# Kernel optimization log

Hardware: AMD Instinct MI355X
Metric: run time of the kernel (lower is better)

The kernel has to match this reference:

```python
import jax, jax.numpy as jnp
import numpy as np

N = 50000       # nodes
E = 800000      # edges
F_IN = 128      # input node features
F_OUT = 16      # per-head output features
H = 8           # attention heads
SLOPE = 0.2     # LeakyReLU negative slope


def setup_inputs() -> dict:
    key = jax.random.key(0)
    k1, k2, k3, k4 = jax.random.split(key, 4)
    node_features = jax.random.normal(k1, (N, F_IN), dtype=jnp.float32)
    edge_index = jax.random.randint(k2, (2, E), 0, N, dtype=jnp.int32)
    # target_w = neighbor_w (share_weights=True): Linear(F_IN -> H*F_OUT) with bias
    W = jax.random.normal(k3, (H * F_OUT, F_IN), dtype=jnp.float32) / np.float32(np.sqrt(F_IN))
    b = jnp.zeros((H * F_OUT,), dtype=jnp.float32)
    # attn = Linear(2*F_OUT -> 1, bias=False); store as vector a of length 2*F_OUT
    a = jax.random.normal(k4, (2 * F_OUT,), dtype=jnp.float32) / np.float32(np.sqrt(2 * F_OUT))
    return {"node_features": node_features, "edge_index": edge_index, "W": W, "b": b, "a": a}


def reference(node_features, edge_index, W, b, a):
    src = edge_index[0]  # neighbor nodes j
    tgt = edge_index[1]  # target nodes i
    # shared projection (share_weights=True): project once per node, then gather per edge
    h = (node_features @ W.T + b).reshape(N, H, F_OUT)  # [N, H, F_OUT]
    h_i = h[tgt]  # [E, H, F_OUT]
    h_j = h[src]  # [E, H, F_OUT]
    # attn applied to concat([h_i, h_j]) == h_i @ a[:F_OUT] + h_j @ a[F_OUT:]
    e = jnp.einsum('ehf,f->eh', h_i, a[:F_OUT]) + jnp.einsum('ehf,f->eh', h_j, a[F_OUT:])
    e = jnp.where(e > 0, e, SLOPE * e)  # LeakyReLU
    # scatter_softmax over incoming edges of each target node (per head)
    seg_max = jax.ops.segment_max(e, tgt, num_segments=N)        # [N, H]
    ex = jnp.exp(e - seg_max[tgt])                               # [E, H]
    denom = jax.ops.segment_sum(ex, tgt, num_segments=N)         # [N, H]
    alpha = ex / denom[tgt]                                      # [E, H]
    # message = alpha * h_j, skip connection adds h_i per edge (as in source)
    msg = alpha[..., None] * h_j + h_i                           # [E, H, F_OUT]
    out = jax.ops.segment_sum(msg, tgt, num_segments=N)          # [N, H, F_OUT]
    out = out.reshape(N, H * F_OUT)                              # concat heads
    return jax.nn.elu(out)
```

## Files before the change

### kernel.cpp

```cpp
#include <hip/hip_runtime.h>
#include <hip/hip_fp16.h>
#include <cmath>

#define NN 50000
#define NE 800000
#define SLOPE 0.2f
#define NTILES 782
#define DSTRIDE 64

#define NBKT 196
#define NCHK 196
#define BINCAP 64

#define OFF_H    0
#define OFF_H8   3200000
#define OFF_AL   4800000
#define OFF_AR   5200000
#define OFF_CUR  5600000
#define OFF_CSR  5650000
#define OFF_BKT  7250000
#define OFF_CNTS 9708624

using half8   = __attribute__((ext_vector_type(8))) _Float16;
using floatx4 = __attribute__((ext_vector_type(4))) float;
using floatx2 = __attribute__((ext_vector_type(2))) float;
using intx4   = __attribute__((ext_vector_type(4))) int;

#define WST 136

__global__ __launch_bounds__(256) void project_bin_kernel(
    const float* __restrict__ X,
    const float* __restrict__ W,
    const float* __restrict__ Bv,
    const float* __restrict__ Av,
    const int* __restrict__ ei,
    __half* __restrict__ h, unsigned char* __restrict__ h8,
    float* __restrict__ al, float* __restrict__ ar,
    unsigned* __restrict__ bkt, unsigned* __restrict__ cnts)
{
    __shared__ _Float16 Wh[128 * WST];
    __shared__ _Float16 Cs[64 * WST];
    __shared__ float As[32];
    __shared__ unsigned bincnt[NBKT];
    const int tid = threadIdx.x;
    const int bid = blockIdx.x;

    if (bid >= NTILES) {
        const int c = bid - NTILES;
        if (tid < NBKT) bincnt[tid] = 0;
        __syncthreads();
#pragma unroll
        for (int it = 0; it < 4; ++it) {
            const int e0 = c * 4096 + tid * 4 + it * 1024;
            if (e0 < NE) {
                intx4 tg = *(const intx4*)(ei + NE + e0);
                intx4 sr = *(const intx4*)(ei + e0);
#pragma unroll
                for (int k = 0; k < 4; ++k) {
                    unsigned p = ((unsigned)tg[k] << 16) | (unsigned)sr[k];
                    unsigned b = p >> 24;
                    unsigned slot = atomicAdd(&bincnt[b], 1u);
                    if (slot < BINCAP)
                        bkt[(((unsigned)c * NBKT + b) << 6) + slot] = p;
                }
            }
        }
        __syncthreads();
        if (tid < NBKT) cnts[c * NBKT + tid] = bincnt[tid];
        return;
    }

    for (int i = tid; i < 128 * 128; i += 256) {
        int o = i >> 7, k = i & 127;
        Wh[o * WST + k] = (_Float16)W[i];
    }
    if (tid < 32) As[tid] = Av[tid];
    __syncthreads();

    const int wave = tid >> 6;
    const int lane = tid & 63;
    const int q = lane >> 4;
    const int n = lane & 15;
    const int gn = bid * 64 + wave * 16 + n;
    const bool valid = gn < NN;
    const float* xrow = X + ((long)gn << 7);

    half8 afrag[4];
#pragma unroll
    for (int kc = 0; kc < 4; ++kc) {
        float4 x0 = make_float4(0.f, 0.f, 0.f, 0.f), x1 = x0;
        if (valid) {
            x0 = *(const float4*)(xrow + kc * 32 + q * 8);
            x1 = *(const float4*)(xrow + kc * 32 + q * 8 + 4);
        }
        half8 a;
        a[0] = (_Float16)x0.x; a[1] = (_Float16)x0.y;
        a[2] = (_Float16)x0.z; a[3] = (_Float16)x0.w;
        a[4] = (_Float16)x1.x; a[5] = (_Float16)x1.y;
        a[6] = (_Float16)x1.z; a[7] = (_Float16)x1.w;
        afrag[kc] = a;
    }

    floatx4 acc[8];
#pragma unroll
    for (int nt = 0; nt < 8; ++nt) {
        float b = Bv[nt * 16 + n];
        acc[nt][0] = b; acc[nt][1] = b; acc[nt][2] = b; acc[nt][3] = b;
    }
#pragma unroll
    for (int nt = 0; nt < 8; ++nt) {
        const _Float16* wrow = &Wh[(nt * 16 + n) * WST];
#pragma unroll
        for (int kc = 0; kc < 4; ++kc) {
            half8 bfrag = *(const half8*)(wrow + kc * 32 + q * 8);
            acc[nt] = __builtin_amdgcn_mfma_f32_16x16x32_f16(afrag[kc], bfrag, acc[nt], 0, 0, 0);
        }
    }

    _Float16* cw = &Cs[(wave * 16) * WST];
#pragma unroll
    for (int nt = 0; nt < 8; ++nt) {
#pragma unroll
        for (int r = 0; r < 4; ++r) {
            cw[(q * 4 + r) * WST + nt * 16 + n] = (_Float16)acc[nt][r];
        }
    }
    __syncthreads();

    {
        int rw = tid >> 2, ch = tid & 3;
        int gnode = bid * 64 + rw;
        if (gnode < NN) {
            const uint4* src = (const uint4*)&Cs[rw * WST + ch * 32];
            uint4 v[4] = { src[0], src[1], src[2], src[3] };
            uint4* dst = (uint4*)&h[((long)gnode << 7) + ch * 32];
            dst[0] = v[0]; dst[1] = v[1]; dst[2] = v[2]; dst[3] = v[3];

            const unsigned int* dw = (const unsigned int*)v;
            unsigned int res[8];
#pragma unroll
            for (int w = 0; w < 8; ++w) {
                unsigned int lo = dw[2 * w], hi = dw[2 * w + 1];
                float2 f0 = __half22float2(*(const __half2*)&lo);
                float2 f1 = __half22float2(*(const __half2*)&hi);
                unsigned int r = 0;
                r = __builtin_amdgcn_cvt_pk_fp8_f32(f0.x, f0.y, r, false);
                r = __builtin_amdgcn_cvt_pk_fp8_f32(f1.x, f1.y, r, true);
                res[w] = r;
            }
            uint4* d8 = (uint4*)&h8[((long)gnode << 7) + ch * 32];
            d8[0] = make_uint4(res[0], res[1], res[2], res[3]);
            d8[1] = make_uint4(res[4], res[5], res[6], res[7]);
        }
    }
    for (int p = tid; p < 512; p += 256) {
        int nd = p >> 3, hh = p & 7;
        int gnode = bid * 64 + nd;
        if (gnode >= NN) continue;
        const _Float16* c = &Cs[nd * WST + hh * 16];
        float pL = 0.f, pR = 0.f;
#pragma unroll
        for (int f = 0; f < 16; ++f) {
            float hv = (float)c[f];
            pL = fmaf(hv, As[f], pL);
            pR = fmaf(hv, As[16 + f], pR);
        }
        al[gnode * 8 + hh] = pL;
        ar[gnode * 8 + hh] = pR;
    }
}

__global__ __launch_bounds__(512) void csr_kernel(
    const unsigned* __restrict__ bkt, const unsigned* __restrict__ cnts,
    int* __restrict__ cur, unsigned short* __restrict__ csr)
{
    __shared__ unsigned short csl[256 * DSTRIDE];
    __shared__ unsigned cnt256[256];
    __shared__ unsigned segcnt[NBKT];
    const int tid = threadIdx.x, bin = blockIdx.x;
    if (tid < 256) cnt256[tid] = 0;
    if (tid < NBKT) segcnt[tid] = cnts[tid * NBKT + bin];
    __syncthreads();

    const int w = tid >> 6, lane = tid & 63;
    for (int s = w; s < NCHK; s += 8) {
        unsigned m = min(segcnt[s], (unsigned)BINCAP);
        if ((unsigned)lane < m) {
            unsigned p = bkt[(((unsigned)s * NBKT + bin) << 6) + lane];
            unsigned local = (p >> 16) & 255u;
            unsigned slot = atomicAdd(&cnt256[local], 1u);
            if (slot < DSTRIDE) csl[(local << 6) + slot] = (unsigned short)(p & 0xFFFFu);
        }
    }
    __syncthreads();

    if (tid < 256) {
        const int gnode = bin * 256 + tid;
        if (gnode < NN) cur[gnode] = (int)cnt256[tid];
    }
    const int nrows = min(256, NN - bin * 256);
    uint4* dst = (uint4*)(csr + ((size_t)bin << 14));
    const uint4* srcp = (const uint4*)csl;
    for (int i = tid; i < nrows * 8; i += 512) dst[i] = srcp[i];
}

#define ARLD(s) (*(const float*)((const char*)ar + ((((unsigned)(s)) << 5) | arof)))
#define CSRLD(o) (*(const unsigned short*)((const char*)csr + (o)))
#define CVTLO(w) __builtin_amdgcn_cvt_pk_f32_fp8((unsigned short)(w), false)
#define CVTHI(w) __builtin_amdgcn_cvt_pk_f32_fp8((unsigned short)((w) >> 16), false)

__global__ __launch_bounds__(256) void gather_kernel(
    const int* __restrict__ cur, const unsigned short* __restrict__ csr,
    const float* __restrict__ al, const float* __restrict__ ar,
    const __half* __restrict__ h, const unsigned char* __restrict__ h8,
    float* __restrict__ out)
{
    const int wid = threadIdx.x >> 6;
    const int n = blockIdx.x * 4 + wid;
    if (n >= NN) return;
    const int lane = threadIdx.x & 63;
    const int c2 = lane << 1;
    const int hh = lane >> 3;
    const int el = lane & 7;
    const int deg = cur[n];
    const int degc = min(deg, DSTRIDE);
    const unsigned cbase = ((unsigned)n) << 7;
    const unsigned arof = ((unsigned)hh) << 2;
    const unsigned hof = ((unsigned)hh) << 4;
    const float aLt = al[n * 8 + hh];

    floatx2 a0 = {0.f,0.f}, a1 = a0, a2 = a0, a3 = a0, a4 = a0, a5 = a0, a6 = a0, a7 = a0;
    float den = 0.f;

    for (int j = 0; j < degc; j += 16) {
        const bool va = (j + el) < degc;
        const bool vb = (j + 8 + el) < degc;
        const unsigned co = cbase + (((unsigned)(j + el)) << 1);
        int ms0 = va ? (int)CSRLD(co) : 0;
        int ms1 = vb ? (int)CSRLD(co + 16u) : 0;
        float v0 = aLt + ARLD(ms0);
        float v1 = aLt + ARLD(ms1);
        v0 = v0 > 0.0f ? v0 : SLOPE * v0;
        v1 = v1 > 0.0f ? v1 : SLOPE * v1;
        float me0 = va ? __expf(fminf(v0, 60.0f)) : 0.0f;
        float me1 = vb ? __expf(fminf(v1, 60.0f)) : 0.0f;
        uint4 A = *(const uint4*)(h8 + ((((unsigned)ms0) << 7) | hof));
        uint4 B = *(const uint4*)(h8 + ((((unsigned)ms1) << 7) | hof));
        den += me0 + me1;
        a0 += CVTLO(A.x) * me0; a1 += CVTHI(A.x) * me0;
        a2 += CVTLO(A.y) * me0; a3 += CVTHI(A.y) * me0;
        a4 += CVTLO(A.z) * me0; a5 += CVTHI(A.z) * me0;
        a6 += CVTLO(A.w) * me0; a7 += CVTHI(A.w) * me0;
        a0 += CVTLO(B.x) * me1; a1 += CVTHI(B.x) * me1;
        a2 += CVTLO(B.y) * me1; a3 += CVTHI(B.y) * me1;
        a4 += CVTLO(B.z) * me1; a5 += CVTHI(B.z) * me1;
        a6 += CVTLO(B.w) * me1; a7 += CVTHI(B.w) * me1;
    }

    {
        floatx2 v0_ = (el & 4) ? a0 : a4;
        floatx2 v1_ = (el & 4) ? a1 : a5;
        floatx2 v2_ = (el & 4) ? a2 : a6;
        floatx2 v3_ = (el & 4) ? a3 : a7;
        floatx2 o0 = (el & 4) ? a4 : a0;
        floatx2 o1 = (el & 4) ? a5 : a1;
        floatx2 o2 = (el & 4) ? a6 : a2;
        floatx2 o3 = (el & 4) ? a7 : a3;
        o0[0] += __shfl_xor(v0_[0], 4); o0[1] += __shfl_xor(v0_[1], 4);
        o1[0] += __shfl_xor(v1_[0], 4); o1[1] += __shfl_xor(v1_[1], 4);
        o2[0] += __shfl_xor(v2_[0], 4); o2[1] += __shfl_xor(v2_[1], 4);
        o3[0] += __shfl_xor(v3_[0], 4); o3[1] += __shfl_xor(v3_[1], 4);
        floatx2 w0 = (el & 2) ? o0 : o2;
        floatx2 w1 = (el & 2) ? o1 : o3;
        floatx2 p0 = (el & 2) ? o2 : o0;
        floatx2 p1 = (el & 2) ? o3 : o1;
        p0[0] += __shfl_xor(w0[0], 2); p0[1] += __shfl_xor(w0[1], 2);
        p1[0] += __shfl_xor(w1[0], 2); p1[1] += __shfl_xor(w1[1], 2);
        floatx2 z = (el & 1) ? p0 : p1;
        floatx2 fin = (el & 1) ? p1 : p0;
        fin[0] += __shfl_xor(z[0], 1); fin[1] += __shfl_xor(z[1], 1);
        a0 = fin;
    }
    den += __shfl_xor(den, 1);
    den += __shfl_xor(den, 2);
    den += __shfl_xor(den, 4);

    unsigned hv = __builtin_nontemporal_load(
        (const unsigned*)((const char*)h + (((size_t)n) << 8) + ((unsigned)c2 << 1)));
    float2 hs = __half22float2(*(const __half2*)&hv);
    float degf = (float)deg;
    float inv = (den > 0.0f) ? 1.0f / den : 0.0f;
    float o0 = fmaf(degf, hs.x, a0[0] * inv);
    float o1 = fmaf(degf, hs.y, a0[1] * inv);
    o0 = o0 > 0.0f ? o0 : __expf(o0) - 1.0f;
    o1 = o1 > 0.0f ? o1 : __expf(o1) - 1.0f;
    floatx2 res = {o0, o1};
    __builtin_nontemporal_store(res,
        (floatx2*)((char*)out + (((size_t)n) << 9) + ((unsigned)c2 << 2)));
}

extern "C" void kernel_launch(void* const* d_in, const int* in_sizes, int n_in,
                              void* d_out, int out_size, void* d_ws, size_t ws_size,
                              hipStream_t stream) {
    const float* X = (const float*)d_in[0];
    const int* ei  = (const int*)d_in[1];
    const float* W = (const float*)d_in[2];
    const float* B = (const float*)d_in[3];
    const float* A = (const float*)d_in[4];
    float* ws  = (float*)d_ws;
    __half* h  = (__half*)(ws + OFF_H);
    unsigned char* h8 = (unsigned char*)(ws + OFF_H8);
    float* al  = ws + OFF_AL;
    float* ar  = ws + OFF_AR;
    int* cur   = (int*)ws + OFF_CUR;
    unsigned short* csr = (unsigned short*)(ws + OFF_CSR);
    unsigned* bkt  = (unsigned*)(ws + OFF_BKT);
    unsigned* cnts = (unsigned*)(ws + OFF_CNTS);
    float* out = (float*)d_out;

    project_bin_kernel<<<NTILES + NCHK, 256, 0, stream>>>(X, W, B, A, ei, h, h8, al, ar, bkt, cnts);
    csr_kernel<<<NBKT, 512, 0, stream>>>(bkt, cnts, cur, csr);
    gather_kernel<<<(NN + 3) / 4, 256, 0, stream>>>(cur, csr, al, ar, h, h8, out);
}
```

Before: 139.6 us.

## Fuse CSR build into gather kernel using shared-memory adjacency per 32-node slice

Merges the CSR construction and gather kernels into one. Each of 8 blocks per 256-node bin rebuilds its 32-node neighbor lists in shared memory, then its waves run the softmax-weighted aggregation straight from LDS. This removes a kernel launch and the global CSR/degree write and read-back. In exchange each bucket entry is read 8 times (once per block in the bin), and each wave handles 8 nodes serially with fewer blocks overall.

```diff
diff --git a/kernel.cpp b/kernel.cpp
--- a/kernel.cpp
+++ b/kernel.cpp
@@ -16,8 +16,6 @@
 #define OFF_H8   3200000
 #define OFF_AL   4800000
 #define OFF_AR   5200000
-#define OFF_CUR  5600000
-#define OFF_CSR  5650000
 #define OFF_BKT  7250000
 #define OFF_CNTS 9708624
 
@@ -170,133 +168,123 @@
     }
 }
 
-__global__ __launch_bounds__(512) void csr_kernel(
+#define ARLD(s) (*(const float*)((const char*)ar + ((((unsigned)(s)) << 5) | arof)))
+#define CVTLO(w) __builtin_amdgcn_cvt_pk_f32_fp8((unsigned short)(w), false)
+#define CVTHI(w) __builtin_amdgcn_cvt_pk_f32_fp8((unsigned short)((w) >> 16), false)
+
+__global__ __launch_bounds__(256) void csr_gather_kernel(
     const unsigned* __restrict__ bkt, const unsigned* __restrict__ cnts,
-    int* __restrict__ cur, unsigned short* __restrict__ csr)
+    const float* __restrict__ al, const float* __restrict__ ar,
+    const __half* __restrict__ h, const unsigned char* __restrict__ h8,
+    float* __restrict__ out)
 {
-    __shared__ unsigned short csl[256 * DSTRIDE];
-    __shared__ unsigned cnt256[256];
+    __shared__ unsigned short csl[32 * DSTRIDE];
+    __shared__ unsigned cnt[32];
     __shared__ unsigned segcnt[NBKT];
-    const int tid = threadIdx.x, bin = blockIdx.x;
-    if (tid < 256) cnt256[tid] = 0;
+    const int tid = threadIdx.x;
+    const int bin = blockIdx.x >> 3;
+    const int o   = blockIdx.x & 7;
+    if (tid < 32) cnt[tid] = 0;
     if (tid < NBKT) segcnt[tid] = cnts[tid * NBKT + bin];
     __syncthreads();
 
     const int w = tid >> 6, lane = tid & 63;
-    for (int s = w; s < NCHK; s += 8) {
+    for (int s = w; s < NCHK; s += 4) {
         unsigned m = min(segcnt[s], (unsigned)BINCAP);
         if ((unsigned)lane < m) {
             unsigned p = bkt[(((unsigned)s * NBKT + bin) << 6) + lane];
             unsigned local = (p >> 16) & 255u;
-            unsigned slot = atomicAdd(&cnt256[local], 1u);
-            if (slot < DSTRIDE) csl[(local << 6) + slot] = (unsigned short)(p & 0xFFFFu);
+            if ((local >> 5) == (unsigned)o) {
+                unsigned idx = local & 31u;
+                unsigned slot = atomicAdd(&cnt[idx], 1u);
+                if (slot < DSTRIDE) csl[(idx << 6) + slot] = (unsigned short)(p & 0xFFFFu);
+            }
         }
     }
     __syncthreads();
 
-    if (tid < 256) {
-        const int gnode = bin * 256 + tid;
-        if (gnode < NN) cur[gnode] = (int)cnt256[tid];
-    }
-    const int nrows = min(256, NN - bin * 256);
-    uint4* dst = (uint4*)(csr + ((size_t)bin << 14));
-    const uint4* srcp = (const uint4*)csl;
-    for (int i = tid; i < nrows * 8; i += 512) dst[i] = srcp[i];
-}
-
-#define ARLD(s) (*(const float*)((const char*)ar + ((((unsigned)(s)) << 5) | arof)))
-#define CSRLD(o) (*(const unsigned short*)((const char*)csr + (o)))
-#define CVTLO(w) __builtin_amdgcn_cvt_pk_f32_fp8((unsigned short)(w), false)
-#define CVTHI(w) __builtin_amdgcn_cvt_pk_f32_fp8((unsigned short)((w) >> 16), false)
-
-__global__ __launch_bounds__(256) void gather_kernel(
-    const int* __restrict__ cur, const unsigned short* __restrict__ csr,
-    const float* __restrict__ al, const float* __restrict__ ar,
-    const __half* __restrict__ h, const unsigned char* __restrict__ h8,
-    float* __restrict__ out)
-{
-    const int wid = threadIdx.x >> 6;
-    const int n = blockIdx.x * 4 + wid;
-    if (n >= NN) return;
-    const int lane = threadIdx.x & 63;
     const int c2 = lane << 1;
     const int hh = lane >> 3;
     const int el = lane & 7;
-    const int deg = cur[n];
-    const int degc = min(deg, DSTRIDE);
-    const unsigned cbase = ((unsigned)n) << 7;
     const unsigned arof = ((unsigned)hh) << 2;
-    const unsigned hof = ((unsigned)hh) << 4;
-    const float aLt = al[n * 8 + hh];
-
-    floatx2 a0 = {0.f,0.f}, a1 = a0, a2 = a0, a3 = a0, a4 = a0, a5 = a0, a6 = a0, a7 = a0;
-    float den = 0.f;
-
-    for (int j = 0; j < degc; j += 16) {
-        const bool va = (j + el) < degc;
-        const bool vb = (j + 8 + el) < degc;
-        const unsigned co = cbase + (((unsigned)(j + el)) << 1);
-        int ms0 = va ? (int)CSRLD(co) : 0;
-        int ms1 = vb ? (int)CSRLD(co + 16u) : 0;
-        float v0 = aLt + ARLD(ms0);
-        float v1 = aLt + ARLD(ms1);
-        v0 = v0 > 0.0f ? v0 : SLOPE * v0;
-        v1 = v1 > 0.0f ? v1 : SLOPE * v1;
-        float me0 = va ? __expf(fminf(v0, 60.0f)) : 0.0f;
-        float me1 = vb ? __expf(fminf(v1, 60.0f)) : 0.0f;
-        uint4 A = *(const uint4*)(h8 + ((((unsigned)ms0) << 7) | hof));
-        uint4 B = *(const uint4*)(h8 + ((((unsigned)ms1) << 7) | hof));
-        den += me0 + me1;
-        a0 += CVTLO(A.x) * me0; a1 += CVTHI(A.x) * me0;
-        a2 += CVTLO(A.y) * me0; a3 += CVTHI(A.y) * me0;
-        a4 += CVTLO(A.z) * me0; a5 += CVTHI(A.z) * me0;
-        a6 += CVTLO(A.w) * me0; a7 += CVTHI(A.w) * me0;
-        a0 += CVTLO(B.x) * me1; a1 += CVTHI(B.x) * me1;
-        a2 += CVTLO(B.y) * me1; a3 += CVTHI(B.y) * me1;
-        a4 += CVTLO(B.z) * me1; a5 += CVTHI(B.z) * me1;
-        a6 += CVTLO(B.w) * me1; a7 += CVTHI(B.w) * me1;
-    }
-
-    {
-        floatx2 v0_ = (el & 4) ? a0 : a4;
-        floatx2 v1_ = (el & 4) ? a1 : a5;
-        floatx2 v2_ = (el & 4) ? a2 : a6;
-        floatx2 v3_ = (el & 4) ? a3 : a7;
-        floatx2 o0 = (el & 4) ? a4 : a0;
-        floatx2 o1 = (el & 4) ? a5 : a1;
-        floatx2 o2 = (el & 4) ? a6 : a2;
-        floatx2 o3 = (el & 4) ? a7 : a3;
-        o0[0] += __shfl_xor(v0_[0], 4); o0[1] += __shfl_xor(v0_[1], 4);
-        o1[0] += __shfl_xor(v1_[0], 4); o1[1] += __shfl_xor(v1_[1], 4);
-        o2[0] += __shfl_xor(v2_[0], 4); o2[1] += __shfl_xor(v2_[1], 4);
-        o3[0] += __shfl_xor(v3_[0], 4); o3[1] += __shfl_xor(v3_[1], 4);
-        floatx2 w0 = (el & 2) ? o0 : o2;
-        floatx2 w1 = (el & 2) ? o1 : o3;
-        floatx2 p0 = (el & 2) ? o2 : o0;
-        floatx2 p1 = (el & 2) ? o3 : o1;
-        p0[0] += __shfl_xor(w0[0], 2); p0[1] += __shfl_xor(w0[1], 2);
-        p1[0] += __shfl_xor(w1[0], 2); p1[1] += __shfl_xor(w1[1], 2);
-        floatx2 z = (el & 1) ? p0 : p1;
-        floatx2 fin = (el & 1) ? p1 : p0;
-        fin[0] += __shfl_xor(z[0], 1); fin[1] += __shfl_xor(z[1], 1);
-        a0 = fin;
-    }
-    den += __shfl_xor(den, 1);
-    den += __shfl_xor(den, 2);
-    den += __shfl_xor(den, 4);
-
-    unsigned hv = __builtin_nontemporal_load(
-        (const unsigned*)((const char*)h + (((size_t)n) << 8) + ((unsigned)c2 << 1)));
-    float2 hs = __half22float2(*(const __half2*)&hv);
-    float degf = (float)deg;
-    float inv = (den > 0.0f) ? 1.0f / den : 0.0f;
-    float o0 = fmaf(degf, hs.x, a0[0] * inv);
-    float o1 = fmaf(degf, hs.y, a0[1] * inv);
-    o0 = o0 > 0.0f ? o0 : __expf(o0) - 1.0f;
-    o1 = o1 > 0.0f ? o1 : __expf(o1) - 1.0f;
-    floatx2 res = {o0, o1};
-    __builtin_nontemporal_store(res,
-        (floatx2*)((char*)out + (((size_t)n) << 9) + ((unsigned)c2 << 2)));
+    const unsigned hof  = ((unsigned)hh) << 4;
+
+    for (int t = 0; t < 8; ++t) {
+        const int idx = w * 8 + t;
+        const int n = bin * 256 + o * 32 + idx;
+        if (n >= NN) break;
+        const int deg = (int)cnt[idx];
+        const int degc = min(deg, DSTRIDE);
+        const float aLt = al[n * 8 + hh];
+        unsigned hv = __builtin_nontemporal_load(
+            (const unsigned*)((const char*)h + (((size_t)n) << 8) + ((unsigned)c2 << 1)));
+        const unsigned short* srcl = &csl[idx << 6];
+
+        floatx2 a0 = {0.f,0.f}, a1 = a0, a2 = a0, a3 = a0, a4 = a0, a5 = a0, a6 = a0, a7 = a0;
+        float den = 0.f;
+        for (int j = 0; j < degc; j += 16) {
+            const bool va = (j + el) < degc;
+            const bool vb = (j + 8 + el) < degc;
+            int ms0 = va ? (int)srcl[j + el] : 0;
+            int ms1 = vb ? (int)srcl[j + 8 + el] : 0;
+            float v0 = aLt + ARLD(ms0);
+            float v1 = aLt + ARLD(ms1);
+            v0 = v0 > 0.0f ? v0 : SLOPE * v0;
+            v1 = v1 > 0.0f ? v1 : SLOPE * v1;
+            float me0 = va ? __expf(fminf(v0, 60.0f)) : 0.0f;
+            float me1 = vb ? __expf(fminf(v1, 60.0f)) : 0.0f;
+            uint4 A = *(const uint4*)(h8 + ((((unsigned)ms0) << 7) | hof));
+            uint4 B = *(const uint4*)(h8 + ((((unsigned)ms1) << 7) | hof));
+            den += me0 + me1;
+            a0 += CVTLO(A.x) * me0; a1 += CVTHI(A.x) * me0;
+            a2 += CVTLO(A.y) * me0; a3 += CVTHI(A.y) * me0;
+            a4 += CVTLO(A.z) * me0; a5 += CVTHI(A.z) * me0;
+            a6 += CVTLO(A.w) * me0; a7 += CVTHI(A.w) * me0;
+            a0 += CVTLO(B.x) * me1; a1 += CVTHI(B.x) * me1;
+            a2 += CVTLO(B.y) * me1; a3 += CVTHI(B.y) * me1;
+            a4 += CVTLO(B.z) * me1; a5 += CVTHI(B.z) * me1;
+            a6 += CVTLO(B.w) * me1; a7 += CVTHI(B.w) * me1;
+        }
+
+        {
+            floatx2 v0_ = (el & 4) ? a0 : a4;
+            floatx2 v1_ = (el & 4) ? a1 : a5;
+            floatx2 v2_ = (el & 4) ? a2 : a6;
+            floatx2 v3_ = (el & 4) ? a3 : a7;
+            floatx2 o0 = (el & 4) ? a4 : a0;
+            floatx2 o1 = (el & 4) ? a5 : a1;
+            floatx2 o2 = (el & 4) ? a6 : a2;
+            floatx2 o3 = (el & 4) ? a7 : a3;
+            o0[0] += __shfl_xor(v0_[0], 4); o0[1] += __shfl_xor(v0_[1], 4);
+            o1[0] += __shfl_xor(v1_[0], 4); o1[1] += __shfl_xor(v1_[1], 4);
+            o2[0] += __shfl_xor(v2_[0], 4); o2[1] += __shfl_xor(v2_[1], 4);
+            o3[0] += __shfl_xor(v3_[0], 4); o3[1] += __shfl_xor(v3_[1], 4);
+            floatx2 w0 = (el & 2) ? o0 : o2;
+            floatx2 w1 = (el & 2) ? o1 : o3;
+            floatx2 p0 = (el & 2) ? o2 : o0;
+            floatx2 p1 = (el & 2) ? o3 : o1;
+            p0[0] += __shfl_xor(w0[0], 2); p0[1] += __shfl_xor(w0[1], 2);
+            p1[0] += __shfl_xor(w1[0], 2); p1[1] += __shfl_xor(w1[1], 2);
+            floatx2 z = (el & 1) ? p0 : p1;
+            floatx2 fin = (el & 1) ? p1 : p0;
+            fin[0] += __shfl_xor(z[0], 1); fin[1] += __shfl_xor(z[1], 1);
+            a0 = fin;
+        }
+        den += __shfl_xor(den, 1);
+        den += __shfl_xor(den, 2);
+        den += __shfl_xor(den, 4);
+
+        float2 hs = __half22float2(*(const __half2*)&hv);
+        float degf = (float)deg;
+        float inv = (den > 0.0f) ? 1.0f / den : 0.0f;
+        float o0v = fmaf(degf, hs.x, a0[0] * inv);
+        float o1v = fmaf(degf, hs.y, a0[1] * inv);
+        o0v = o0v > 0.0f ? o0v : __expf(o0v) - 1.0f;
+        o1v = o1v > 0.0f ? o1v : __expf(o1v) - 1.0f;
+        floatx2 res = {o0v, o1v};
+        __builtin_nontemporal_store(res,
+            (floatx2*)((char*)out + (((size_t)n) << 9) + ((unsigned)c2 << 2)));
+    }
 }
 
 extern "C" void kernel_launch(void* const* d_in, const int* in_sizes, int n_in,
@@ -312,13 +300,10 @@
     unsigned char* h8 = (unsigned char*)(ws + OFF_H8);
     float* al  = ws + OFF_AL;
     float* ar  = ws + OFF_AR;
-    int* cur   = (int*)ws + OFF_CUR;
-    unsigned short* csr = (unsigned short*)(ws + OFF_CSR);
     unsigned* bkt  = (unsigned*)(ws + OFF_BKT);
     unsigned* cnts = (unsigned*)(ws + OFF_CNTS);
     float* out = (float*)d_out;
 
     project_bin_kernel<<<NTILES + NCHK, 256, 0, stream>>>(X, W, B, A, ei, h, h8, al, ar, bkt, cnts);
-    csr_kernel<<<NBKT, 512, 0, stream>>>(bkt, cnts, cur, csr);
-    gather_kernel<<<(NN + 3) / 4, 256, 0, stream>>>(cur, csr, al, ar, h, h8, out);
+    csr_gather_kernel<<<NBKT * 8, 256, 0, stream>>>(bkt, cnts, al, ar, h, h8, out);
 }
```

Result: slower. 151.8 us (+8.8%).
